# Performance work log

Measured on AMD Instinct MI355X. Metric: run time of the kernel, lower is better.

## Reference

```python
import jax, jax.numpy as jnp
import numpy as np

N, E, D, H, ED = 50000, 800000, 64, 8, 16
DH = D // H  # 8


def setup_inputs() -> dict:
    key = jax.random.key(0)
    ks = jax.random.split(key, 16)
    s = 0.05
    return {
        "x": jax.random.normal(ks[0], (N, D), jnp.float32),
        "edge_index": jax.random.randint(ks[1], (2, E), 0, N, jnp.int32),
        "edge_attr": jax.random.normal(ks[2], (E, ED), jnp.float32),
        "Wq": jax.random.normal(ks[3], (D, D), jnp.float32) * s,
        "bq": jnp.zeros((D,), jnp.float32),
        "Wk": jax.random.normal(ks[4], (D, D), jnp.float32) * s,
        "bk": jnp.zeros((D,), jnp.float32),
        "Wv": jax.random.normal(ks[5], (D, D), jnp.float32) * s,
        "bv": jnp.zeros((D,), jnp.float32),
        "We": jax.random.normal(ks[6], (ED, D), jnp.float32) * s,
        "be": jnp.zeros((D,), jnp.float32),
        "Wskip": jax.random.normal(ks[7], (D, D), jnp.float32) * s,
        "bskip": jnp.zeros((D,), jnp.float32),
        "Wbeta": jax.random.normal(ks[8], (3 * D, 1), jnp.float32) * s,
        "gamma": jnp.ones((D,), jnp.float32),
        "beta_bn": jnp.zeros((D,), jnp.float32),
    }


def reference(x, edge_index, edge_attr, Wq, bq, Wk, bk, Wv, bv, We, be,
              Wskip, bskip, Wbeta, gamma, beta_bn):
    n, d = x.shape
    src, dst = edge_index[0], edge_index[1]
    # per-node projections, then gather per edge (PyG TransformerConv)
    q = (x @ Wq + bq).reshape(n, H, DH)
    k = (x @ Wk + bk).reshape(n, H, DH)
    v = (x @ Wv + bv).reshape(n, H, DH)
    e = (edge_attr @ We + be).reshape(-1, H, DH)
    ke = k[src] + e                      # [E,H,DH]
    ve = v[src] + e                      # [E,H,DH]
    logits = (q[dst] * ke).sum(-1) / jnp.sqrt(jnp.float32(DH))  # [E,H]
    # segment softmax over incoming edges of each destination node
    m = jax.ops.segment_max(logits, dst, num_segments=n)
    p = jnp.exp(logits - m[dst])
    denom = jax.ops.segment_sum(p, dst, num_segments=n)
    alpha = p / (denom[dst] + 1e-16)     # [E,H]
    out = jax.ops.segment_sum(alpha[:, :, None] * ve, dst, num_segments=n)
    out = out.reshape(n, d)              # concat heads
    # beta-gated skip connection (beta=True, root_weight=True)
    x_r = x @ Wskip + bskip
    g = jax.nn.sigmoid(jnp.concatenate([out, x_r, out - x_r], axis=-1) @ Wbeta)
    out = g * x_r + (1.0 - g) * out
    # BatchNorm1d (training forward: batch statistics), eps=1e-5
    mean = out.mean(axis=0)
    var = out.var(axis=0)
    out = (out - mean) * jax.lax.rsqrt(var + 1e-5) * gamma + beta_bn
    # LeakyReLU(0.01); dropout is identity in eval
    return jnp.where(out >= 0, out, 0.01 * out)
```

## Files before the change

### kernel.cpp

```cpp
#include <hip/hip_runtime.h>

#define D   64
#define H   8
#define DH  8
#define ED  16
#define QK_SCALE 0.35355339059327373f

typedef unsigned int uint_t;

__device__ __forceinline__ void fma4(float4& a, float s, const float4& w) {
    a.x += s * w.x; a.y += s * w.y; a.z += s * w.z; a.w += s * w.w;
}
__device__ __forceinline__ uint_t f2bf(float f) {
    uint_t u = __float_as_uint(f);
    return (u + 0x7FFFu + ((u >> 16) & 1u)) >> 16;
}
__device__ __forceinline__ float bf_lo(uint_t u) { return __uint_as_float(u << 16); }
__device__ __forceinline__ float bf_hi(uint_t u) { return __uint_as_float(u & 0xFFFF0000u); }

__device__ __forceinline__ float khreduce8(const float* acc, int e) {
    int b0 = e & 1, b1 = (e >> 1) & 1, b2 = (e >> 2) & 1;
    float t0[4];
    #pragma unroll
    for (int j = 0; j < 4; ++j) {
        float k = b0 ? acc[2*j+1] : acc[2*j];
        float s = b0 ? acc[2*j]   : acc[2*j+1];
        t0[j] = k + __shfl_xor(s, 8);
    }
    float t1[2];
    #pragma unroll
    for (int j = 0; j < 2; ++j) {
        float k = b1 ? t0[2*j+1] : t0[2*j];
        float s = b1 ? t0[2*j]   : t0[2*j+1];
        t1[j] = k + __shfl_xor(s, 16);
    }
    float k = b2 ? t1[1] : t1[0];
    float s = b2 ? t1[0] : t1[1];
    return k + __shfl_xor(s, 32);
}

__global__ __launch_bounds__(256) void proj_qs_hist(
    const float* __restrict__ x,
    const float* __restrict__ Wq, const float* __restrict__ bq,
    const float* __restrict__ Ws, const float* __restrict__ bs,
    const float* __restrict__ We, const float* __restrict__ be,
    uint_t* __restrict__ qxr,
    uint_t* __restrict__ Ap, float* __restrict__ qbe, int N,
    const int* __restrict__ ei, int* __restrict__ cnt, int E, int projBlocks)
{
    __shared__ float sW[2][D * D];
    __shared__ float sWe[ED * D];
    __shared__ float sbe[D];
    if (blockIdx.x >= projBlocks) {
        int gid = (blockIdx.x - projBlocks) * 256 + threadIdx.x;
        if (gid < E) atomicAdd(&cnt[ei[E + gid]], 1);
        return;
    }
    {
        for (int t = threadIdx.x; t < D * D; t += 256) {
            sW[0][t] = Wq[t];
            sW[1][t] = Ws[t];
        }
        for (int t = threadIdx.x; t < ED * D; t += 256) sWe[t] = We[t];
        if (threadIdx.x < D) sbe[threadIdx.x] = be[threadIdx.x];
    }
    __syncthreads();

    int cg = (threadIdx.x & 15) * 4;
    float4 vbq = *(const float4*)(bq + cg);
    float4 vbs = *(const float4*)(bs + cg);
    int h  = cg >> 3;
    int hh = (cg >> 2) & 1;

    #pragma unroll 1
    for (int it = 0; it < 4; ++it) {
        int node = blockIdx.x * 64 + it * 16 + (threadIdx.x >> 4);
        if (node >= N) return;

        float4 aq = {0,0,0,0}, as_ = {0,0,0,0};
        const float* xrow = x + (size_t)node * D;

        #pragma unroll
        for (int i = 0; i < D; i += 4) {
            float4 xv = *(const float4*)(xrow + i);
            #pragma unroll
            for (int s = 0; s < 4; ++s) {
                float xs = (&xv.x)[s];
                fma4(aq,  xs, *(const float4*)(&sW[0][(i + s) * D + cg]));
                fma4(as_, xs, *(const float4*)(&sW[1][(i + s) * D + cg]));
            }
        }
        aq.x = (aq.x + vbq.x) * QK_SCALE;
        aq.y = (aq.y + vbq.y) * QK_SCALE;
        aq.z = (aq.z + vbq.z) * QK_SCALE;
        aq.w = (aq.w + vbq.w) * QK_SCALE;
        as_.x += vbs.x; as_.y += vbs.y; as_.z += vbs.z; as_.w += vbs.w;

        uint4 pqx;
        pqx.x = f2bf(aq.x) | (f2bf(as_.x) << 16);
        pqx.y = f2bf(aq.y) | (f2bf(as_.y) << 16);
        pqx.z = f2bf(aq.z) | (f2bf(as_.z) << 16);
        pqx.w = f2bf(aq.w) | (f2bf(as_.w) << 16);
        *(uint4*)(qxr + (size_t)node * D + cg) = pqx;

        float part[ED];
        #pragma unroll
        for (int i = 0; i < ED; ++i) {
            float4 we4 = *(const float4*)(&sWe[i * D + cg]);
            part[i] = aq.x * we4.x + aq.y * we4.y + aq.z * we4.z + aq.w * we4.w;
        }
        float4 be4 = *(const float4*)(&sbe[cg]);
        float qb = aq.x * be4.x + aq.y * be4.y + aq.z * be4.z + aq.w * be4.w;
        #pragma unroll
        for (int i = 0; i < ED; ++i) part[i] += __shfl_xor(part[i], 1);
        qb += __shfl_xor(qb, 1);

        uint4 apk;
        apk.x = f2bf(part[hh * 8 + 0]) | (f2bf(part[hh * 8 + 1]) << 16);
        apk.y = f2bf(part[hh * 8 + 2]) | (f2bf(part[hh * 8 + 3]) << 16);
        apk.z = f2bf(part[hh * 8 + 4]) | (f2bf(part[hh * 8 + 5]) << 16);
        apk.w = f2bf(part[hh * 8 + 6]) | (f2bf(part[hh * 8 + 7]) << 16);
        *(uint4*)(Ap + (size_t)node * 64 + h * 8 + hh * 4) = apk;
        if (hh == 0) qbe[(size_t)node * 8 + h] = qb;
    }
}

__global__ __launch_bounds__(256) void proj_kv_scana(
    const float* __restrict__ x,
    const float* __restrict__ Wk, const float* __restrict__ bk,
    const float* __restrict__ Wv, const float* __restrict__ bv,
    uint_t* __restrict__ kvp, int N, int kvBlocks,
    const int* __restrict__ cnt, int* __restrict__ bsum)
{
    __shared__ float sW[2][D * D];
    __shared__ int red[256];
    if (blockIdx.x >= kvBlocks) {
        int t = threadIdx.x;
        int i = (blockIdx.x - kvBlocks) * 256 + t;
        red[t] = (i < N) ? cnt[i] : 0;
        __syncthreads();
        for (int s = 128; s > 0; s >>= 1) {
            if (t < s) red[t] += red[t + s];
            __syncthreads();
        }
        if (t == 0) bsum[blockIdx.x - kvBlocks] = red[0];
        return;
    }
    for (int t = threadIdx.x; t < D * D; t += 256) {
        sW[0][t] = Wk[t];
        sW[1][t] = Wv[t];
    }
    __syncthreads();

    int cg = (threadIdx.x & 15) * 4;
    float4 vbk = *(const float4*)(bk + cg);
    float4 vbv = *(const float4*)(bv + cg);

    #pragma unroll 1
    for (int it = 0; it < 4; ++it) {
        int node = blockIdx.x * 64 + it * 16 + (threadIdx.x >> 4);
        if (node >= N) return;

        float4 ak = {0,0,0,0}, av = {0,0,0,0};
        const float* xrow = x + (size_t)node * D;

        #pragma unroll
        for (int i = 0; i < D; i += 4) {
            float4 xv = *(const float4*)(xrow + i);
            #pragma unroll
            for (int s = 0; s < 4; ++s) {
                float xs = (&xv.x)[s];
                fma4(ak, xs, *(const float4*)(&sW[0][(i + s) * D + cg]));
                fma4(av, xs, *(const float4*)(&sW[1][(i + s) * D + cg]));
            }
        }
        ak.x += vbk.x; ak.y += vbk.y; ak.z += vbk.z; ak.w += vbk.w;
        av.x += vbv.x; av.y += vbv.y; av.z += vbv.z; av.w += vbv.w;

        uint4 pkv;
        pkv.x = f2bf(ak.x) | (f2bf(av.x) << 16);
        pkv.y = f2bf(ak.y) | (f2bf(av.y) << 16);
        pkv.z = f2bf(ak.z) | (f2bf(av.z) << 16);
        pkv.w = f2bf(ak.w) | (f2bf(av.w) << 16);
        *(uint4*)(kvp + (size_t)node * D + cg) = pkv;
    }
}

__global__ __launch_bounds__(256) void scan_c(
    const int* __restrict__ cnt, const int* __restrict__ bsum,
    int* __restrict__ row_start, int* __restrict__ cursor, int N, int E, int nb)
{
    __shared__ int sb[256];
    __shared__ int sh[256];
    int t = threadIdx.x;
    int bv = (t < nb) ? bsum[t] : 0;
    sb[t] = bv;
    __syncthreads();
    for (int s = 1; s < 256; s <<= 1) {
        int a = (t >= s) ? sb[t - s] : 0;
        __syncthreads();
        sb[t] += a;
        __syncthreads();
    }
    int boff = sb[blockIdx.x] - bsum[blockIdx.x];

    int i = blockIdx.x * 256 + t;
    int v = (i < N) ? cnt[i] : 0;
    sh[t] = v;
    __syncthreads();
    for (int s = 1; s < 256; s <<= 1) {
        int a = (t >= s) ? sh[t - s] : 0;
        __syncthreads();
        sh[t] += a;
        __syncthreads();
    }
    int excl = sh[t] - v + boff;
    if (i < N) { row_start[i] = excl; cursor[i] = excl; }
    if (i == N - 1) row_start[N] = E;
}

__global__ __launch_bounds__(256) void csr_scatter(
    const int* __restrict__ ei, const float4* __restrict__ ea4,
    int* __restrict__ cursor, int* __restrict__ srcs_s,
    uint_t* __restrict__ ea_s, int E)
{
    int gid = blockIdx.x * 256 + threadIdx.x;
    if (gid >= E) return;
    int src = ei[gid];
    int dst = ei[E + gid];
    float4 r0 = ea4[(size_t)gid * 4 + 0];
    float4 r1 = ea4[(size_t)gid * 4 + 1];
    float4 r2 = ea4[(size_t)gid * 4 + 2];
    float4 r3 = ea4[(size_t)gid * 4 + 3];
    int pos = atomicAdd(&cursor[dst], 1);
    srcs_s[pos] = src;
    uint4 p0, p1;
    p0.x = f2bf(r0.x) | (f2bf(r0.y) << 16);
    p0.y = f2bf(r0.z) | (f2bf(r0.w) << 16);
    p0.z = f2bf(r1.x) | (f2bf(r1.y) << 16);
    p0.w = f2bf(r1.z) | (f2bf(r1.w) << 16);
    p1.x = f2bf(r2.x) | (f2bf(r2.y) << 16);
    p1.y = f2bf(r2.z) | (f2bf(r2.w) << 16);
    p1.z = f2bf(r3.x) | (f2bf(r3.y) << 16);
    p1.w = f2bf(r3.z) | (f2bf(r3.w) << 16);
    *(uint4*)(ea_s + (size_t)pos * 8)     = p0;
    *(uint4*)(ea_s + (size_t)pos * 8 + 4) = p1;
}

__global__ __launch_bounds__(256, 4) void node_gather(
    const int*   __restrict__ row_start,
    const int*   __restrict__ srcs_s,
    const uint_t* __restrict__ ea_s,
    const float* __restrict__ We, const float* __restrict__ be,
    const uint_t* __restrict__ qxr, const uint_t* __restrict__ kvp,
    const uint_t* __restrict__ Ap, const float* __restrict__ qbe,
    const float* __restrict__ Wbeta,
    float* __restrict__ out, float* __restrict__ S1p, float* __restrict__ S2p,
    int N)
{
    __shared__ float l1[4][D];
    __shared__ float l2[4][D];
    int lane = threadIdx.x & 63;
    int w    = threadIdx.x >> 6;
    int h    = lane & 7;
    int e    = lane >> 3;
    int cmix = h * 8 + e;

    float w0[8], w1[8];
    #pragma unroll
    for (int j = 0; j < 8; ++j) {
        w0[j] = We[(2 * e)     * D + h * 8 + j];
        w1[j] = We[(2 * e + 1) * D + h * 8 + j];
    }
    float bev = be[cmix];
    float wb0 = Wbeta[cmix], wb1 = Wbeta[D + cmix], wb2 = Wbeta[2 * D + cmix];

    float s1bn = 0.f, s2bn = 0.f;
    int stride = gridDim.x * 4;

    for (int nid = blockIdx.x * 4 + w; nid < N; nid += stride) {
        int rs  = row_start[nid];
        int deg = row_start[nid + 1] - rs;

        const uint4* qxp = (const uint4*)(qxr + (size_t)nid * D + h * 8);
        uint4 qx0 = qxp[0], qx1 = qxp[1];
        float q8[8];
        q8[0] = bf_lo(qx0.x); q8[1] = bf_lo(qx0.y);
        q8[2] = bf_lo(qx0.z); q8[3] = bf_lo(qx0.w);
        q8[4] = bf_lo(qx1.x); q8[5] = bf_lo(qx1.y);
        q8[6] = bf_lo(qx1.z); q8[7] = bf_lo(qx1.w);
        uint_t xru0 = (e & 2) ? ((e & 1) ? qx0.w : qx0.z)
                              : ((e & 1) ? qx0.y : qx0.x);
        uint_t xru1 = (e & 2) ? ((e & 1) ? qx1.w : qx1.z)
                              : ((e & 1) ? qx1.y : qx1.x);
        float xrv = bf_hi((e & 4) ? xru1 : xru0);

        const uint4* app = (const uint4*)(Ap + (size_t)nid * 64 + h * 8);
        uint4 au0 = app[0], au1 = app[1];
        float a16[ED];
        #pragma unroll
        for (int j = 0; j < 4; ++j) {
            a16[j * 2]         = bf_lo((&au0.x)[j]);
            a16[j * 2 + 1]     = bf_hi((&au0.x)[j]);
            a16[8 + j * 2]     = bf_lo((&au1.x)[j]);
            a16[8 + j * 2 + 1] = bf_hi((&au1.x)[j]);
        }
        float qbeh = qbe[(size_t)nid * 8 + h];

        float acc[8] = {0,0,0,0,0,0,0,0};
        float sv[ED] = {0,0,0,0,0,0,0,0,0,0,0,0,0,0,0,0};
        float den = 0.f;

        int src_next = (e < deg) ? srcs_s[rs + e] : 0;

        for (int j0 = 0; j0 < deg; j0 += 8) {
            int src = src_next;
            {
                int enx = j0 + 8 + e;
                src_next = (enx < deg) ? srcs_s[rs + enx] : 0;
            }
            int eidx = j0 + e;
            bool valid = eidx < deg;
            int ce = valid ? eidx : 0;

            const uint4* kp = (const uint4*)(kvp + (size_t)src * 64 + h * 8);
            uint4 k0 = kp[0], k1 = kp[1];
            const uint4* ep = (const uint4*)(ea_s + (size_t)(rs + ce) * 8);
            uint4 u0 = ep[0], u1 = ep[1];

            float ex[ED];
            #pragma unroll
            for (int j = 0; j < 4; ++j) {
                ex[j * 2]         = bf_lo((&u0.x)[j]);
                ex[j * 2 + 1]     = bf_hi((&u0.x)[j]);
                ex[8 + j * 2]     = bf_lo((&u1.x)[j]);
                ex[8 + j * 2 + 1] = bf_hi((&u1.x)[j]);
            }
            float c = qbeh;
            c += q8[0] * bf_lo(k0.x); c += q8[1] * bf_lo(k0.y);
            c += q8[2] * bf_lo(k0.z); c += q8[3] * bf_lo(k0.w);
            c += q8[4] * bf_lo(k1.x); c += q8[5] * bf_lo(k1.y);
            c += q8[6] * bf_lo(k1.z); c += q8[7] * bf_lo(k1.w);
            #pragma unroll
            for (int i = 0; i < ED; ++i) c += ex[i] * a16[i];

            float p = valid ? __expf(c) : 0.f;
            den += p;
            acc[0] += p * bf_hi(k0.x); acc[1] += p * bf_hi(k0.y);
            acc[2] += p * bf_hi(k0.z); acc[3] += p * bf_hi(k0.w);
            acc[4] += p * bf_hi(k1.x); acc[5] += p * bf_hi(k1.y);
            acc[6] += p * bf_hi(k1.z); acc[7] += p * bf_hi(k1.w);
            #pragma unroll
            for (int i = 0; i < ED; ++i) sv[i] += p * ex[i];
        }

        den += __shfl_xor(den, 8);
        den += __shfl_xor(den, 16);
        den += __shfl_xor(den, 32);

        float u[8];
        #pragma unroll
        for (int j = 0; j < 8; ++j) {
            int i0 = ((j & 6) << 1) | (j & 1);
            float k = (e & 1) ? sv[i0 | 2] : sv[i0];
            float s = (e & 1) ? sv[i0] : sv[i0 | 2];
            u[j] = k + __shfl_xor(s, 8);
        }
        float v2[4];
        #pragma unroll
        for (int j = 0; j < 4; ++j) {
            int j0 = ((j & 2) << 1) | (j & 1);
            float k = (e & 2) ? u[j0 | 2] : u[j0];
            float s = (e & 2) ? u[j0] : u[j0 | 2];
            v2[j] = k + __shfl_xor(s, 16);
        }
        float S0, S1;
        {
            float k0 = (e & 4) ? v2[2] : v2[0];
            float s0 = (e & 4) ? v2[0] : v2[2];
            S0 = k0 + __shfl_xor(s0, 32);
            float k1 = (e & 4) ? v2[3] : v2[1];
            float s1 = (e & 4) ? v2[1] : v2[3];
            S1 = k1 + __shfl_xor(s1, 32);
        }

        float cj[8];
        #pragma unroll
        for (int j = 0; j < 8; ++j) cj[j] = S0 * w0[j] + S1 * w1[j];
        float esum = khreduce8(cj, e);
        float vsum = khreduce8(acc, e);

        float o = (vsum + esum + bev * den) / (den + 1e-16f);

        float tb  = o * wb0 + xrv * wb1 + (o - xrv) * wb2;
        #pragma unroll
        for (int s = 1; s < 64; s <<= 1) tb += __shfl_xor(tb, s);
        float g  = 1.f / (1.f + __expf(-tb));
        float o2 = g * xrv + (1.f - g) * o;
        out[(size_t)nid * D + cmix] = o2;
        s1bn += o2; s2bn += o2 * o2;
    }

    l1[w][cmix] = s1bn; l2[w][cmix] = s2bn;
    __syncthreads();
    if (threadIdx.x < D) {
        float a = l1[0][threadIdx.x] + l1[1][threadIdx.x]
                + l1[2][threadIdx.x] + l1[3][threadIdx.x];
        float b = l2[0][threadIdx.x] + l2[1][threadIdx.x]
                + l2[2][threadIdx.x] + l2[3][threadIdx.x];
        unsafeAtomicAdd(&S1p[threadIdx.x * 64], a);
        unsafeAtomicAdd(&S2p[threadIdx.x * 64], b);
    }
}

__global__ __launch_bounds__(256) void bn_apply(
    float4* __restrict__ out, const float* __restrict__ S1p,
    const float* __restrict__ S2p, const float* __restrict__ gamma,
    const float* __restrict__ beta, int total4, float invN)
{
    int gid = blockIdx.x * 256 + threadIdx.x;
    if (gid >= total4) return;
    int col = (gid & 15) * 4;
    float4 g4 = *(const float4*)(gamma + col);
    float4 b4 = *(const float4*)(beta + col);
    float4 y  = out[gid];
    #pragma unroll
    for (int j = 0; j < 4; ++j) {
        float mean = S1p[(col + j) * 64] * invN;
        float var  = S2p[(col + j) * 64] * invN - mean * mean;
        float sc   = (&g4.x)[j] * rsqrtf(var + 1e-5f);
        float sh   = (&b4.x)[j] - mean * sc;
        float tv   = (&y.x)[j] * sc + sh;
        (&y.x)[j]  = (tv >= 0.f) ? tv : 0.01f * tv;
    }
    out[gid] = y;
}

extern "C" void kernel_launch(void* const* d_in, const int* in_sizes, int n_in,
                              void* d_out, int out_size, void* d_ws, size_t ws_size,
                              hipStream_t stream)
{
    const float* x     = (const float*)d_in[0];
    const int*   ei    = (const int*)  d_in[1];
    const float* ea    = (const float*)d_in[2];
    const float* Wq    = (const float*)d_in[3];
    const float* bq    = (const float*)d_in[4];
    const float* Wk    = (const float*)d_in[5];
    const float* bk    = (const float*)d_in[6];
    const float* Wv    = (const float*)d_in[7];
    const float* bv    = (const float*)d_in[8];
    const float* We    = (const float*)d_in[9];
    const float* be    = (const float*)d_in[10];
    const float* Wskip = (const float*)d_in[11];
    const float* bskip = (const float*)d_in[12];
    const float* Wbeta = (const float*)d_in[13];
    const float* gamma = (const float*)d_in[14];
    const float* betab = (const float*)d_in[15];

    int N = in_sizes[0] / D;
    int E = in_sizes[1] / 2;

    int*    ws        = (int*)d_ws;
    int*    cnt       = ws;
    float*  S1p       = (float*)(ws + 50000);
    float*  S2p       = (float*)(ws + 54096);
    int*    row_start = ws + 58192;
    int*    bsum      = ws + 108240;
    int*    srcs_s    = ws + 108544;
    uint_t* ea_s      = (uint_t*)(ws + 908544);
    uint_t* kvp       = (uint_t*)(ws + 7308544);
    uint_t* qxr       = (uint_t*)(ws + 10508544);
    uint_t* Ap        = (uint_t*)(ws + 13708544);
    float*  qbe       = (float*)(ws + 16908544);

    hipMemsetAsync(d_ws, 0, (size_t)58192 * sizeof(int), stream);

    int projB = (N + 63) / 64;
    int histB = (E + 255) / 256;
    proj_qs_hist<<<projB + histB, 256, 0, stream>>>(
        x, Wq, bq, Wskip, bskip, We, be,
        qxr, Ap, qbe, N, ei, cnt, E, projB);

    int scanB = (N + 255) / 256;
    proj_kv_scana<<<projB + scanB, 256, 0, stream>>>(
        x, Wk, bk, Wv, bv, kvp, N, projB, cnt, bsum);

    scan_c<<<scanB, 256, 0, stream>>>(cnt, bsum, row_start, cnt, N, E, scanB);

    csr_scatter<<<(E + 255) / 256, 256, 0, stream>>>(
        ei, (const float4*)ea, cnt, srcs_s, ea_s, E);

    node_gather<<<1024, 256, 0, stream>>>(
        row_start, srcs_s, ea_s, We, be, qxr, kvp, Ap, qbe, Wbeta,
        (float*)d_out, S1p, S2p, N);

    bn_apply<<<(N * 16 + 255) / 256, 256, 0, stream>>>(
        (float4*)d_out, S1p, S2p, gamma, betab, N * 16, 1.0f / (float)N);
}
```

Baseline: 204.6 us.

## Compute K/V projection with bf16 MFMA and persistent wave tiling

Replaces the scalar FP32 FMA K/V projection, which staged weights through shared memory, with bf16 MFMA 16x16x32 instructions. Each wave keeps the weight fragments in registers and loops persistently over 16-node tiles, using a fixed grid of 196 blocks. Inputs are now rounded to bf16 before the multiply, which slightly reduces precision. Output stores are 4-byte scattered writes instead of uint4, which may lower store efficiency. N is a multiple of 16, so there is no tail guard.

```diff
diff --git a/kernel.cpp b/kernel.cpp
--- a/kernel.cpp
+++ b/kernel.cpp
@@ -7,6 +7,8 @@
 #define QK_SCALE 0.35355339059327373f
 
 typedef unsigned int uint_t;
+typedef __attribute__((ext_vector_type(8))) short bf16x8;
+typedef __attribute__((ext_vector_type(4))) float f32x4;
 
 __device__ __forceinline__ void fma4(float4& a, float s, const float4& w) {
     a.x += s * w.x; a.y += s * w.y; a.z += s * w.z; a.w += s * w.w;
@@ -132,7 +134,6 @@
     uint_t* __restrict__ kvp, int N, int kvBlocks,
     const int* __restrict__ cnt, int* __restrict__ bsum)
 {
-    __shared__ float sW[2][D * D];
     __shared__ int red[256];
     if (blockIdx.x >= kvBlocks) {
         int t = threadIdx.x;
@@ -146,43 +147,60 @@
         if (t == 0) bsum[blockIdx.x - kvBlocks] = red[0];
         return;
     }
-    for (int t = threadIdx.x; t < D * D; t += 256) {
-        sW[0][t] = Wk[t];
-        sW[1][t] = Wv[t];
-    }
-    __syncthreads();
-
-    int cg = (threadIdx.x & 15) * 4;
-    float4 vbk = *(const float4*)(bk + cg);
-    float4 vbv = *(const float4*)(bv + cg);
-
-    #pragma unroll 1
-    for (int it = 0; it < 4; ++it) {
-        int node = blockIdx.x * 64 + it * 16 + (threadIdx.x >> 4);
-        if (node >= N) return;
-
-        float4 ak = {0,0,0,0}, av = {0,0,0,0};
-        const float* xrow = x + (size_t)node * D;
-
-        #pragma unroll
-        for (int i = 0; i < D; i += 4) {
-            float4 xv = *(const float4*)(xrow + i);
+
+    int lane = threadIdx.x & 63;
+    int wv   = threadIdx.x >> 6;
+    int l = lane & 15, g = lane >> 4;
+
+    bf16x8 Bf[2][4][2];
+    #pragma unroll
+    for (int ct = 0; ct < 4; ++ct)
+        #pragma unroll
+        for (int kh = 0; kh < 2; ++kh)
             #pragma unroll
-            for (int s = 0; s < 4; ++s) {
-                float xs = (&xv.x)[s];
-                fma4(ak, xs, *(const float4*)(&sW[0][(i + s) * D + cg]));
-                fma4(av, xs, *(const float4*)(&sW[1][(i + s) * D + cg]));
+            for (int j = 0; j < 8; ++j) {
+                int k = kh * 32 + g * 8 + j;
+                int c = ct * 16 + l;
+                Bf[0][ct][kh][j] = (short)f2bf(Wk[k * 64 + c]);
+                Bf[1][ct][kh][j] = (short)f2bf(Wv[k * 64 + c]);
             }
-        }
-        ak.x += vbk.x; ak.y += vbk.y; ak.z += vbk.z; ak.w += vbk.w;
-        av.x += vbv.x; av.y += vbv.y; av.z += vbv.z; av.w += vbv.w;
-
-        uint4 pkv;
-        pkv.x = f2bf(ak.x) | (f2bf(av.x) << 16);
-        pkv.y = f2bf(ak.y) | (f2bf(av.y) << 16);
-        pkv.z = f2bf(ak.z) | (f2bf(av.z) << 16);
-        pkv.w = f2bf(ak.w) | (f2bf(av.w) << 16);
-        *(uint4*)(kvp + (size_t)node * D + cg) = pkv;
+    float bkc[4], bvc[4];
+    #pragma unroll
+    for (int ct = 0; ct < 4; ++ct) {
+        bkc[ct] = bk[ct * 16 + l];
+        bvc[ct] = bv[ct * 16 + l];
+    }
+
+    int nt   = (N + 15) >> 4;
+    int wtot = kvBlocks * 4;
+    for (int t = blockIdx.x * 4 + wv; t < nt; t += wtot) {
+        int n0 = t * 16;
+        bf16x8 Af[2];
+        const float* xr = x + (size_t)(n0 + l) * 64 + g * 8;
+        #pragma unroll
+        for (int kh = 0; kh < 2; ++kh) {
+            float4 p0 = *(const float4*)(xr + kh * 32);
+            float4 p1 = *(const float4*)(xr + kh * 32 + 4);
+            Af[kh][0] = (short)f2bf(p0.x); Af[kh][1] = (short)f2bf(p0.y);
+            Af[kh][2] = (short)f2bf(p0.z); Af[kh][3] = (short)f2bf(p0.w);
+            Af[kh][4] = (short)f2bf(p1.x); Af[kh][5] = (short)f2bf(p1.y);
+            Af[kh][6] = (short)f2bf(p1.z); Af[kh][7] = (short)f2bf(p1.w);
+        }
+        #pragma unroll
+        for (int ct = 0; ct < 4; ++ct) {
+            f32x4 ck = {0.f, 0.f, 0.f, 0.f};
+            f32x4 cv = {0.f, 0.f, 0.f, 0.f};
+            ck = __builtin_amdgcn_mfma_f32_16x16x32_bf16(Af[0], Bf[0][ct][0], ck, 0, 0, 0);
+            ck = __builtin_amdgcn_mfma_f32_16x16x32_bf16(Af[1], Bf[0][ct][1], ck, 0, 0, 0);
+            cv = __builtin_amdgcn_mfma_f32_16x16x32_bf16(Af[0], Bf[1][ct][0], cv, 0, 0, 0);
+            cv = __builtin_amdgcn_mfma_f32_16x16x32_bf16(Af[1], Bf[1][ct][1], cv, 0, 0, 0);
+            #pragma unroll
+            for (int r = 0; r < 4; ++r) {
+                int node = n0 + g * 4 + r;
+                uint_t pk = f2bf(ck[r] + bkc[ct]) | (f2bf(cv[r] + bvc[ct]) << 16);
+                kvp[(size_t)node * 64 + ct * 16 + l] = pk;
+            }
+        }
     }
 }
 
@@ -482,8 +500,9 @@
         qxr, Ap, qbe, N, ei, cnt, E, projB);
 
     int scanB = (N + 255) / 256;
-    proj_kv_scana<<<projB + scanB, 256, 0, stream>>>(
-        x, Wk, bk, Wv, bv, kvp, N, projB, cnt, bsum);
+    int kvB   = 196;
+    proj_kv_scana<<<kvB + scanB, 256, 0, stream>>>(
+        x, Wk, bk, Wv, bv, kvp, N, kvB, cnt, bsum);
 
     scan_c<<<scanB, 256, 0, stream>>>(cnt, bsum, row_start, cnt, N, E, scanB);
 
```

Result: faster. 189.9 us, median of 3 (-7.2%).
